# Kernel optimization log

Measured on AMD Instinct MI355X. Metric: run time of the kernel, lower is better.

## Reference

```python
import jax, jax.numpy as jnp
import numpy as np

BATCH, SEQ_LEN, EMBED_DIM = 32, 2048, 128
N_QLAYERS = 2
N_WIRES = 18  # ceil(log2(128*2048)) ; 2**18 == 128*2048 exactly


def rot_matrices(p):
    # p: [n_wires, 3] (phi, theta, omega) -> [n_wires, 2, 2] complex64
    # PennyLane/torchquantum Rot convention: RZ(omega) RY(theta) RZ(phi)
    phi, th, om = p[..., 0], p[..., 1], p[..., 2]
    c, s = jnp.cos(th / 2), jnp.sin(th / 2)
    e = lambda a: jnp.exp(1j * a)  # float32 -> complex64 (weak complex scalar)
    m00 = e(-(phi + om) / 2) * c
    m01 = -e((phi - om) / 2) * s
    m10 = e(-(phi - om) / 2) * s
    m11 = e((phi + om) / 2) * c
    return jnp.stack([jnp.stack([m00, m01], -1), jnp.stack([m10, m11], -1)], -2)


def apply_1q(state, U, w):
    # state: [B, 2^n] complex; wire 0 is the most-significant qubit axis
    B = state.shape[0]
    L, R = 2 ** w, 2 ** (N_WIRES - 1 - w)
    s = state.reshape(B, L, 2, R)
    s = jnp.einsum('ij,bljr->blir', U, s)
    return s.reshape(B, -1)


def apply_cnot(state, c, t):
    # flip target bit t where control bit c == 1
    B = state.shape[0]
    s = state.reshape((B,) + (2,) * N_WIRES)
    ca, ta = c + 1, t + 1
    s0 = jnp.take(s, 0, axis=ca)
    s1 = jnp.take(s, 1, axis=ca)
    flip_axis = ta - 1 if ta > ca else ta  # target axis index after removing control axis
    s1 = jnp.flip(s1, axis=flip_axis)
    return jnp.stack([s0, s1], axis=ca).reshape(B, -1)


def setup_inputs() -> dict:
    key = jax.random.key(0)
    k1, k2 = jax.random.split(key)
    x = jax.random.normal(k1, (BATCH, SEQ_LEN, EMBED_DIM), dtype=jnp.float32)
    params = jax.random.uniform(k2, (N_QLAYERS, N_WIRES, 3), dtype=jnp.float32,
                                minval=-np.pi, maxval=np.pi)
    return {"x": x, "params": params}


def reference(x, params):
    B = x.shape[0]
    v = x.reshape(B, -1)
    # StateEncoder: L2-normalize amplitudes (2^N_WIRES == SEQ_LEN*EMBED_DIM, no padding needed)
    v = v / jnp.sqrt(jnp.sum(v * v, axis=-1, keepdims=True))
    state = v.astype(jnp.complex64)
    for l in range(N_QLAYERS):
        U = rot_matrices(params[l])  # [N_WIRES, 2, 2]
        for w in range(N_WIRES):
            state = apply_1q(state, U[w], w)
        for i in range(N_WIRES):
            state = apply_cnot(state, (i + l) % N_WIRES, (i + l + 1) % N_WIRES)
    return jnp.abs(state).reshape(B, SEQ_LEN, EMBED_DIM)
```

## Files before the change

kernel.cpp:

```cpp
#include <hip/hip_runtime.h>
#include <hip/hip_fp16.h>

#define NW 18
#define NSTATE (1u << NW)
#define NBATCH 32
#define TOTAL (NBATCH * (size_t)NSTATE)

typedef float v2f __attribute__((ext_vector_type(2)));
typedef _Float16 h2v __attribute__((ext_vector_type(2)));

struct Masks { unsigned m[18]; };

__device__ __forceinline__ v2f pk_mulsw(v2f g, v2f b) {
    v2f d;
    asm("v_pk_mul_f32 %0, %1, %2 op_sel:[1,1] op_sel_hi:[1,0] neg_lo:[1,0]"
        : "=v"(d) : "v"(g), "v"(b));
    return d;
}
__device__ __forceinline__ v2f pk_fmare(v2f g, v2f a, v2f c) {
    v2f d;
    asm("v_pk_fma_f32 %0, %1, %2, %3 op_sel:[0,0,0] op_sel_hi:[0,1,1]"
        : "=v"(d) : "v"(g), "v"(a), "v"(c));
    return d;
}
__device__ __forceinline__ v2f pk_fmasw(v2f g, v2f a, v2f c) {
    v2f d;
    asm("v_pk_fma_f32 %0, %1, %2, %3 op_sel:[1,1,0] op_sel_hi:[1,0,1] neg_lo:[1,0,0]"
        : "=v"(d) : "v"(g), "v"(a), "v"(c));
    return d;
}
__device__ __forceinline__ v2f cmul(v2f g, v2f x) { return pk_fmare(g, x, pk_mulsw(g, x)); }
__device__ __forceinline__ v2f cmad(v2f g, v2f x, v2f c) { return pk_fmare(g, x, pk_fmasw(g, x, c)); }

__device__ __forceinline__ void bfly(v2f& a, v2f& b, v2f g00, v2f g01, v2f g10, v2f g11) {
    v2f na = cmad(g00, a, cmul(g01, b));
    v2f nb = cmad(g10, a, cmul(g11, b));
    a = na; b = nb;
}

__device__ __forceinline__ unsigned pack(v2f v) {
    return __builtin_bit_cast(unsigned, __builtin_amdgcn_cvt_pkrtz(v.x, v.y));
}
__device__ __forceinline__ v2f unpack(unsigned u) {
    h2v h = __builtin_bit_cast(h2v, u);
    return (v2f){(float)h.x, (float)h.y};
}

__device__ __forceinline__ int swz(int n) { return n ^ ((n >> 5) & 31); }

__device__ __forceinline__ constexpr int ctzc(int x) {
    int c = 0; while (!(x & 1)) { x >>= 1; c++; } return c;
}

#define GATES(gb)                                                      \
    const float4 G0_ = Ut[(17-(gb))*2+0], G1_ = Ut[(17-(gb))*2+1];     \
    const v2f g00 = {G0_.x, G0_.y}, g01 = {G0_.z, G0_.w};              \
    const v2f g10 = {G1_.x, G1_.y}, g11 = {G1_.z, G1_.w};

__device__ __forceinline__ void make_gate(const float* __restrict__ p,
                                          float4& G0, float4& G1) {
    float phi = p[0], th = p[1], om = p[2];
    float ch = cosf(th*0.5f), sh = sinf(th*0.5f);
    float a0 = -0.5f*(phi+om), a1 = 0.5f*(phi-om);
    float c0 = cosf(a0), s0 = sinf(a0);
    float c1 = cosf(a1), s1 = sinf(a1);
    G0 = make_float4(c0*ch,  s0*ch, -c1*sh, -s1*sh);
    G1 = make_float4(c1*sh, -s1*sh,  c0*ch, -s0*ch);
}

template<int FIRST>
__global__ __launch_bounds__(256, 6) void passA(const void* __restrict__ src,
                                                unsigned* __restrict__ dst,
                                                float4* __restrict__ Utab,
                                                float* __restrict__ partials,
                                                const float* __restrict__ params,
                                                int layer) {
    __shared__ unsigned sm[4096];
    __shared__ float4 gl[72];
    __shared__ float wsum[4];
    const int t = threadIdx.x;
    const size_t base = (size_t)blockIdx.x * 4096;
    v2f v[16];
    const float4* Ut;
    float ss = 0.f;

    if (FIRST) {
        const float4* xs = (const float4*)((const float*)src + base + (size_t)t * 16);

        if (t < 36) {
            float4 G0, G1;
            make_gate(params + t*3, G0, G1);
            gl[t*2] = G0; gl[t*2+1] = G1;
            if (blockIdx.x == 0) { Utab[t*2] = G0; Utab[t*2+1] = G1; }
        }

#pragma unroll
        for (int j = 0; j < 4; j++) {
            float4 q = xs[j];
            v[j*4+0] = (v2f){q.x, 0.f};
            v[j*4+1] = (v2f){q.y, 0.f};
            v[j*4+2] = (v2f){q.z, 0.f};
            v[j*4+3] = (v2f){q.w, 0.f};
            ss += q.x*q.x + q.y*q.y + q.z*q.z + q.w*q.w;
        }
#pragma unroll
        for (int m = 32; m >= 1; m >>= 1) ss += __shfl_xor(ss, m, 64);
        if ((t & 63) == 0) wsum[t >> 6] = ss;
        __syncthreads();
        Ut = gl;
    } else {
        const uint4* xs = (const uint4*)((const unsigned*)src + base + (size_t)t * 16);
#pragma unroll
        for (int j = 0; j < 4; j++) {
            uint4 q = xs[j];
            v[j*4+0] = unpack(q.x);
            v[j*4+1] = unpack(q.y);
            v[j*4+2] = unpack(q.z);
            v[j*4+3] = unpack(q.w);
        }
        Ut = (const float4*)Utab + (size_t)layer * 36;
    }

#pragma unroll
    for (int b = 0; b < 4; b++) {
        GATES(b);
#pragma unroll
        for (int k = 0; k < 16; k++)
            if (!(k & (1 << b))) bfly(v[k], v[k | (1 << b)], g00, g01, g10, g11);
    }

#pragma unroll
    for (int k = 0; k < 16; k++)
        sm[swz((t << 4) | k)] = pack(v[k]);
    __syncthreads();
    if (FIRST && t == 0)
        partials[blockIdx.x] = wsum[0] + wsum[1] + wsum[2] + wsum[3];
#pragma unroll
    for (int k = 0; k < 16; k++)
        v[k] = unpack(sm[swz((t & 15) | (k << 4) | ((t >> 4) << 8))]);

#pragma unroll
    for (int b = 4; b < 8; b++) {
        GATES(b);
        const int pb = 1 << (b - 4);
#pragma unroll
        for (int k = 0; k < 16; k++)
            if (!(k & pb)) bfly(v[k], v[k | pb], g00, g01, g10, g11);
    }

#pragma unroll
    for (int k = 0; k < 16; k++)
        sm[swz((t & 15) | (k << 4) | ((t >> 4) << 8))] = pack(v[k]);
    __syncthreads();
#pragma unroll
    for (int k = 0; k < 16; k++)
        v[k] = unpack(sm[swz(t | (k << 8))]);

#pragma unroll
    for (int b = 8; b < 12; b++) {
        GATES(b);
        const int pb = 1 << (b - 8);
#pragma unroll
        for (int k = 0; k < 16; k++)
            if (!(k & pb)) bfly(v[k], v[k | pb], g00, g01, g10, g11);
    }

#pragma unroll
    for (int k = 0; k < 16; k++)
        dst[base + (t | (k << 8))] = pack(v[k]);
}

template<int LAST>
__global__ __launch_bounds__(256, 6) void passB(const unsigned* __restrict__ src,
                                                void* __restrict__ dst,
                                                const float4* __restrict__ Utab,
                                                const float* __restrict__ partials,
                                                int layer, Masks mk) {
    __shared__ unsigned sm[4096];
    const int t = threadIdx.x;
    const unsigned blk = blockIdx.x;
    const unsigned batch = blk >> 6;
    const unsigned chunk = blk & 63;
    const unsigned low = chunk * 64 + (t & 63);
    const unsigned j = t >> 6;
    const size_t bb = (size_t)batch << NW;

    v2f v[16];
#pragma unroll
    for (int k = 0; k < 16; k++) {
        unsigned h = (j << 4) | k;
        v[k] = unpack(src[bb + ((size_t)h << 12) + low]);
    }

    const float4* Ut = Utab + (size_t)layer * 36;
#pragma unroll
    for (int b = 12; b < 16; b++) {
        GATES(b);
        const int pb = 1 << (b - 12);
#pragma unroll
        for (int k = 0; k < 16; k++)
            if (!(k & pb)) bfly(v[k], v[k | pb], g00, g01, g10, g11);
    }

#pragma unroll
    for (int k = 0; k < 16; k++) {
        unsigned h = (j << 4) | k;
        sm[(h << 6) | (t & 63)] = pack(v[k]);
    }
    __syncthreads();
#pragma unroll
    for (int q = 0; q < 4; q++)
#pragma unroll
        for (int r = 0; r < 4; r++) {
            unsigned h = (q << 4) | (j << 2) | r;
            v[(q << 2) | r] = unpack(sm[(h << 6) | (t & 63)]);
        }

    {
        GATES(16);
#pragma unroll
        for (int k = 0; k < 16; k++)
            if (!(k & 4)) bfly(v[k], v[k | 4], g00, g01, g10, g11);
    }
    {
        GATES(17);
#pragma unroll
        for (int k = 0; k < 16; k++)
            if (!(k & 8)) bfly(v[k], v[k | 8], g00, g01, g10, g11);
    }

    unsigned f = 0;
#pragma unroll
    for (int kk = 0; kk < 12; kk++) f ^= ((low >> kk) & 1u) ? mk.m[kk] : 0u;
    if (j & 1) f ^= mk.m[14];
    if (j & 2) f ^= mk.m[15];

    float sc = 1.f;
    if (LAST) {
        float nrm = 0.f;
#pragma unroll
        for (int i = 0; i < 64; i++) nrm += partials[batch * 64 + i];
        sc = rsqrtf(nrm);
    }

    const unsigned gm0 = mk.m[12], gm1 = mk.m[13], gm2 = mk.m[16], gm3 = mk.m[17];
    unsigned fs = f;
#pragma unroll
    for (int i = 0; i < 16; i++) {
        if (i) {
            const int c = ctzc(i);
            fs ^= (c == 0) ? gm0 : (c == 1) ? gm1 : (c == 2) ? gm2 : gm3;
        }
        const int s = i ^ (i >> 1);
        if (LAST) {
            ((float*)dst)[bb + fs] = sc * sqrtf(fmaf(v[s].x, v[s].x, v[s].y*v[s].y));
        } else {
            ((unsigned*)dst)[bb + fs] = pack(v[s]);
        }
    }
}

static void chain_masks(int l, Masks* mk) {
    unsigned rows[18];
    for (int j = 0; j < 18; j++) rows[j] = 1u << j;
    for (int i = 0; i < 18; i++) {
        int cw = (i + l) % 18, tw = (i + l + 1) % 18;
        rows[17 - tw] ^= rows[17 - cw];
    }
    for (int k = 0; k < 18; k++) {
        unsigned cm = 0;
        for (int j = 0; j < 18; j++) cm |= ((rows[j] >> k) & 1u) << j;
        mk->m[k] = cm;
    }
}

extern "C" void kernel_launch(void* const* d_in, const int* in_sizes, int n_in,
                              void* d_out, int out_size, void* d_ws, size_t ws_size,
                              hipStream_t stream) {
    const float* x      = (const float*)d_in[0];
    const float* params = (const float*)d_in[1];

    char* ws = (char*)d_ws;
    unsigned* bufA  = (unsigned*)ws;
    unsigned* bufB  = (unsigned*)(ws + TOTAL * 4);
    float4*   Utab  = (float4*)(ws + TOTAL * 8);
    float* partials = (float*)(ws + TOTAL * 8 + 4096);

    Masks mk1, mk2;
    chain_masks(0, &mk1);
    chain_masks(1, &mk2);

    passA<1><<<2048, 256, 0, stream>>>((const void*)x, bufA, Utab, partials, params, 0);
    passB<0><<<2048, 256, 0, stream>>>(bufA, (void*)bufB, Utab, partials, 0, mk1);
    passA<0><<<2048, 256, 0, stream>>>((const void*)bufB, bufB, Utab, partials, params, 1);
    passB<1><<<2048, 256, 0, stream>>>(bufB, d_out, Utab, partials, 1, mk2);
}
```

Measured before the change: 157.9 us.

## Fuse quantum circuit into three passes by commuting CNOT permutation across layer-2 gates

Reorganises the two-layer circuit from four kernels into three. Layer 1's high-wire gates and some of layer 2's gates now run in one middle pass, with the CNOT-chain permutation folded into gate-pair selection through parity-dependent gate swaps and a prefix-XOR index remap. A final pass applies the remaining layer-2 gates, applies the combined permutation, and writes magnitudes. This removes one full read and write of the fp16-packed state, at the cost of more complex index arithmetic, runtime gate selection, and a lower occupancy hint in the launch bounds.

```diff
diff --git a/kernel.cpp b/kernel.cpp
--- a/kernel.cpp
+++ b/kernel.cpp
@@ -10,6 +10,7 @@
 typedef _Float16 h2v __attribute__((ext_vector_type(2)));
 
 struct Masks { unsigned m[18]; };
+struct G4 { v2f a, b, c, d; };
 
 __device__ __forceinline__ v2f pk_mulsw(v2f g, v2f b) {
     v2f d;
@@ -32,10 +33,22 @@
 __device__ __forceinline__ v2f cmul(v2f g, v2f x) { return pk_fmare(g, x, pk_mulsw(g, x)); }
 __device__ __forceinline__ v2f cmad(v2f g, v2f x, v2f c) { return pk_fmare(g, x, pk_fmasw(g, x, c)); }
 
-__device__ __forceinline__ void bfly(v2f& a, v2f& b, v2f g00, v2f g01, v2f g10, v2f g11) {
-    v2f na = cmad(g00, a, cmul(g01, b));
-    v2f nb = cmad(g10, a, cmul(g11, b));
-    a = na; b = nb;
+__device__ __forceinline__ void bflyG(v2f& x, v2f& y, const G4 g) {
+    v2f nx = cmad(g.a, x, cmul(g.b, y));
+    v2f ny = cmad(g.c, x, cmul(g.d, y));
+    x = nx; y = ny;
+}
+
+__device__ __forceinline__ G4 loadg(const float4* __restrict__ Ut, int gb) {
+    float4 G0 = Ut[(17 - gb) * 2], G1 = Ut[(17 - gb) * 2 + 1];
+    G4 g; g.a = (v2f){G0.x, G0.y}; g.b = (v2f){G0.z, G0.w};
+    g.c = (v2f){G1.x, G1.y}; g.d = (v2f){G1.z, G1.w};
+    return g;
+}
+__device__ __forceinline__ G4 selg(const G4 g, unsigned p) {
+    G4 r; r.a = p ? g.d : g.a; r.b = p ? g.c : g.b;
+    r.c = p ? g.b : g.c; r.d = p ? g.a : g.d;
+    return r;
 }
 
 __device__ __forceinline__ unsigned pack(v2f v) {
@@ -47,107 +60,93 @@
 }
 
 __device__ __forceinline__ int swz(int n) { return n ^ ((n >> 5) & 31); }
+#define SWZ2(L) ((unsigned)(L) ^ (((((unsigned)(L)) >> 5) ^ (((unsigned)(L)) >> 6)) & 1u))
 
 __device__ __forceinline__ constexpr int ctzc(int x) {
     int c = 0; while (!(x & 1)) { x >>= 1; c++; } return c;
 }
-
-#define GATES(gb)                                                      \
-    const float4 G0_ = Ut[(17-(gb))*2+0], G1_ = Ut[(17-(gb))*2+1];     \
-    const v2f g00 = {G0_.x, G0_.y}, g01 = {G0_.z, G0_.w};              \
-    const v2f g10 = {G1_.x, G1_.y}, g11 = {G1_.z, G1_.w};
+__device__ __forceinline__ unsigned pfx18(unsigned x) {
+    x ^= x << 1; x ^= x << 2; x ^= x << 4; x ^= x << 8; x ^= x << 16;
+    return x & 0x3FFFFu;
+}
 
 __device__ __forceinline__ void make_gate(const float* __restrict__ p,
                                           float4& G0, float4& G1) {
     float phi = p[0], th = p[1], om = p[2];
-    float ch = cosf(th*0.5f), sh = sinf(th*0.5f);
-    float a0 = -0.5f*(phi+om), a1 = 0.5f*(phi-om);
+    float ch = cosf(th * 0.5f), sh = sinf(th * 0.5f);
+    float a0 = -0.5f * (phi + om), a1 = 0.5f * (phi - om);
     float c0 = cosf(a0), s0 = sinf(a0);
     float c1 = cosf(a1), s1 = sinf(a1);
-    G0 = make_float4(c0*ch,  s0*ch, -c1*sh, -s1*sh);
-    G1 = make_float4(c1*sh, -s1*sh,  c0*ch, -s0*ch);
-}
-
-template<int FIRST>
-__global__ __launch_bounds__(256, 6) void passA(const void* __restrict__ src,
+    G0 = make_float4(c0 * ch, s0 * ch, -c1 * sh, -s1 * sh);
+    G1 = make_float4(c1 * sh, -s1 * sh, c0 * ch, -s0 * ch);
+}
+
+__global__ __launch_bounds__(256, 4) void pass1(const float* __restrict__ src,
                                                 unsigned* __restrict__ dst,
                                                 float4* __restrict__ Utab,
                                                 float* __restrict__ partials,
-                                                const float* __restrict__ params,
-                                                int layer) {
+                                                const float* __restrict__ params) {
     __shared__ unsigned sm[4096];
-    __shared__ float4 gl[72];
+    __shared__ float4 gl[36];
     __shared__ float wsum[4];
     const int t = threadIdx.x;
     const size_t base = (size_t)blockIdx.x * 4096;
     v2f v[16];
-    const float4* Ut;
     float ss = 0.f;
 
-    if (FIRST) {
-        const float4* xs = (const float4*)((const float*)src + base + (size_t)t * 16);
-
-        if (t < 36) {
-            float4 G0, G1;
-            make_gate(params + t*3, G0, G1);
-            gl[t*2] = G0; gl[t*2+1] = G1;
-            if (blockIdx.x == 0) { Utab[t*2] = G0; Utab[t*2+1] = G1; }
+    const float4* xs = (const float4*)(src + base + (size_t)t * 16);
+
+    if (t < 36) {
+        float4 G0, G1; make_gate(params + t * 3, G0, G1);
+        if (t < 18) { gl[t * 2] = G0; gl[t * 2 + 1] = G1; }
+        if (blockIdx.x == 0) {
+            Utab[t * 2] = G0; Utab[t * 2 + 1] = G1;
+            if (t >= 18) {
+                Utab[72 + (t - 18) * 2 + 0] = make_float4(G1.z, G1.w, G1.x, G1.y);
+                Utab[72 + (t - 18) * 2 + 1] = make_float4(G0.z, G0.w, G0.x, G0.y);
+            }
         }
-
-#pragma unroll
-        for (int j = 0; j < 4; j++) {
-            float4 q = xs[j];
-            v[j*4+0] = (v2f){q.x, 0.f};
-            v[j*4+1] = (v2f){q.y, 0.f};
-            v[j*4+2] = (v2f){q.z, 0.f};
-            v[j*4+3] = (v2f){q.w, 0.f};
-            ss += q.x*q.x + q.y*q.y + q.z*q.z + q.w*q.w;
-        }
-#pragma unroll
-        for (int m = 32; m >= 1; m >>= 1) ss += __shfl_xor(ss, m, 64);
-        if ((t & 63) == 0) wsum[t >> 6] = ss;
-        __syncthreads();
-        Ut = gl;
-    } else {
-        const uint4* xs = (const uint4*)((const unsigned*)src + base + (size_t)t * 16);
-#pragma unroll
-        for (int j = 0; j < 4; j++) {
-            uint4 q = xs[j];
-            v[j*4+0] = unpack(q.x);
-            v[j*4+1] = unpack(q.y);
-            v[j*4+2] = unpack(q.z);
-            v[j*4+3] = unpack(q.w);
-        }
-        Ut = (const float4*)Utab + (size_t)layer * 36;
-    }
+    }
+
+#pragma unroll
+    for (int j = 0; j < 4; j++) {
+        float4 q = xs[j];
+        v[j * 4 + 0] = (v2f){q.x, 0.f};
+        v[j * 4 + 1] = (v2f){q.y, 0.f};
+        v[j * 4 + 2] = (v2f){q.z, 0.f};
+        v[j * 4 + 3] = (v2f){q.w, 0.f};
+        ss += q.x * q.x + q.y * q.y + q.z * q.z + q.w * q.w;
+    }
+#pragma unroll
+    for (int m = 32; m >= 1; m >>= 1) ss += __shfl_xor(ss, m, 64);
+    if ((t & 63) == 0) wsum[t >> 6] = ss;
+    __syncthreads();
+
+    const float4* Ut = gl;
 
 #pragma unroll
     for (int b = 0; b < 4; b++) {
-        GATES(b);
-#pragma unroll
-        for (int k = 0; k < 16; k++)
-            if (!(k & (1 << b))) bfly(v[k], v[k | (1 << b)], g00, g01, g10, g11);
-    }
-
+        G4 g = loadg(Ut, b);
+#pragma unroll
+        for (int k = 0; k < 16; k++)
+            if (!(k & (1 << b))) bflyG(v[k], v[k | (1 << b)], g);
+    }
 #pragma unroll
     for (int k = 0; k < 16; k++)
         sm[swz((t << 4) | k)] = pack(v[k]);
     __syncthreads();
-    if (FIRST && t == 0)
-        partials[blockIdx.x] = wsum[0] + wsum[1] + wsum[2] + wsum[3];
+    if (t == 0) partials[blockIdx.x] = wsum[0] + wsum[1] + wsum[2] + wsum[3];
 #pragma unroll
     for (int k = 0; k < 16; k++)
         v[k] = unpack(sm[swz((t & 15) | (k << 4) | ((t >> 4) << 8))]);
-
 #pragma unroll
     for (int b = 4; b < 8; b++) {
-        GATES(b);
+        G4 g = loadg(Ut, b);
         const int pb = 1 << (b - 4);
 #pragma unroll
         for (int k = 0; k < 16; k++)
-            if (!(k & pb)) bfly(v[k], v[k | pb], g00, g01, g10, g11);
-    }
-
+            if (!(k & pb)) bflyG(v[k], v[k | pb], g);
+    }
 #pragma unroll
     for (int k = 0; k < 16; k++)
         sm[swz((t & 15) | (k << 4) | ((t >> 4) << 8))] = pack(v[k]);
@@ -155,122 +154,231 @@
 #pragma unroll
     for (int k = 0; k < 16; k++)
         v[k] = unpack(sm[swz(t | (k << 8))]);
-
 #pragma unroll
     for (int b = 8; b < 12; b++) {
-        GATES(b);
+        G4 g = loadg(Ut, b);
         const int pb = 1 << (b - 8);
 #pragma unroll
         for (int k = 0; k < 16; k++)
-            if (!(k & pb)) bfly(v[k], v[k | pb], g00, g01, g10, g11);
-    }
-
+            if (!(k & pb)) bflyG(v[k], v[k | pb], g);
+    }
 #pragma unroll
     for (int k = 0; k < 16; k++)
         dst[base + (t | (k << 8))] = pack(v[k]);
 }
 
-template<int LAST>
-__global__ __launch_bounds__(256, 6) void passB(const unsigned* __restrict__ src,
-                                                void* __restrict__ dst,
-                                                const float4* __restrict__ Utab,
-                                                const float* __restrict__ partials,
-                                                int layer, Masks mk) {
+__global__ __launch_bounds__(256, 4) void pass2(const unsigned* __restrict__ src,
+                                                unsigned* __restrict__ dst,
+                                                const float4* __restrict__ Utab) {
     __shared__ unsigned sm[4096];
     const int t = threadIdx.x;
     const unsigned blk = blockIdx.x;
-    const unsigned batch = blk >> 6;
-    const unsigned chunk = blk & 63;
-    const unsigned low = chunk * 64 + (t & 63);
-    const unsigned j = t >> 6;
+    const unsigned batch = blk >> 6, chunk = blk & 63;
     const size_t bb = (size_t)batch << NW;
-
+    const int lane6 = t & 63, j2 = t >> 6;
+    const float4* Ut0  = Utab;
+    const float4* Ut1  = Utab + 36;
+    const float4* Ut1s = Utab + 72;
     v2f v[16];
+
+#pragma unroll
+    for (int k = 0; k < 16; k++)
+        v[k] = unpack(src[bb + ((size_t)((j2 << 4) | k) << 12) + (chunk << 6) + lane6]);
+
+#pragma unroll
+    for (int b = 0; b < 4; b++) {
+        G4 g = loadg(Ut0, 12 + b);
+#pragma unroll
+        for (int k = 0; k < 16; k++)
+            if (!(k & (1 << b))) bflyG(v[k], v[k | (1 << b)], g);
+    }
+
+#pragma unroll
+    for (int k = 0; k < 16; k++)
+        sm[SWZ2((((j2 << 4) | k) << 6) | lane6)] = pack(v[k]);
+    __syncthreads();
+    const int l5 = t & 31, m3 = t >> 5;
 #pragma unroll
     for (int k = 0; k < 16; k++) {
-        unsigned h = (j << 4) | k;
-        v[k] = unpack(src[bb + ((size_t)h << 12) + low]);
-    }
-
-    const float4* Ut = Utab + (size_t)layer * 36;
-#pragma unroll
-    for (int b = 12; b < 16; b++) {
-        GATES(b);
-        const int pb = 1 << (b - 12);
-#pragma unroll
-        for (int k = 0; k < 16; k++)
-            if (!(k & pb)) bfly(v[k], v[k | pb], g00, g01, g10, g11);
-    }
+        int L = ((((k >> 3) << 5) | (((k >> 2) & 1) << 4) | (((k >> 1) & 1) << 3) | m3) << 6)
+                | (l5 << 1) | (k & 1);
+        v[k] = unpack(sm[SWZ2(L)]);
+    }
+
+    { G4 g = loadg(Ut0, 16);
+#pragma unroll
+      for (int k = 0; k < 16; k++) if (!(k & 4)) bflyG(v[k], v[k | 4], g); }
+    { G4 g = loadg(Ut0, 17);
+#pragma unroll
+      for (int k = 0; k < 16; k++) if (!(k & 8)) bflyG(v[k], v[k | 8], g); }
+
+    { G4 g = loadg(Ut1, 16);
+#pragma unroll
+      for (int k = 0; k < 16; k++) if (!(k & 2)) {
+          const int q = k ^ 6, pe = ((k >> 2) ^ (k >> 3)) & 1;
+          if (pe) bflyG(v[q], v[k], g); else bflyG(v[k], v[q], g);
+      } }
+
+    const unsigned ptv = (unsigned)((__popc(l5) + __popc((int)chunk) + __popc(m3)) & 1);
+
+    { G4 gn = loadg(Ut1, 17);
+      G4 cA = selg(gn, ptv), cB = selg(gn, ptv ^ 1u);
+#pragma unroll
+      for (int k = 0; k < 16; k++) if (!(k & 4)) {
+          const int q = k ^ 12, pe = (k ^ (k >> 1) ^ (k >> 2)) & 1;
+          bflyG(v[k], v[q], pe ? cB : cA);
+      } }
+
+    { G4 gn = loadg(Ut1, 0);
+      G4 cA = selg(gn, ptv), cB = selg(gn, ptv ^ 1u);
+#pragma unroll
+      for (int k = 0; k < 16; k++) if (!(k & 1)) {
+          const int q = k ^ 13, pe = (k ^ (k >> 1) ^ (k >> 2) ^ (k >> 3)) & 1;
+          bflyG(v[k], v[q], pe ? cB : cA);
+      } }
 
 #pragma unroll
     for (int k = 0; k < 16; k++) {
-        unsigned h = (j << 4) | k;
-        sm[(h << 6) | (t & 63)] = pack(v[k]);
-    }
-    __syncthreads();
-#pragma unroll
-    for (int q = 0; q < 4; q++)
-#pragma unroll
-        for (int r = 0; r < 4; r++) {
-            unsigned h = (q << 4) | (j << 2) | r;
-            v[(q << 2) | r] = unpack(sm[(h << 6) | (t & 63)]);
-        }
-
-    {
-        GATES(16);
-#pragma unroll
-        for (int k = 0; k < 16; k++)
-            if (!(k & 4)) bfly(v[k], v[k | 4], g00, g01, g10, g11);
-    }
-    {
-        GATES(17);
-#pragma unroll
-        for (int k = 0; k < 16; k++)
-            if (!(k & 8)) bfly(v[k], v[k | 8], g00, g01, g10, g11);
-    }
-
-    unsigned f = 0;
-#pragma unroll
-    for (int kk = 0; kk < 12; kk++) f ^= ((low >> kk) & 1u) ? mk.m[kk] : 0u;
-    if (j & 1) f ^= mk.m[14];
-    if (j & 2) f ^= mk.m[15];
-
-    float sc = 1.f;
-    if (LAST) {
-        float nrm = 0.f;
-#pragma unroll
-        for (int i = 0; i < 64; i++) nrm += partials[batch * 64 + i];
-        sc = rsqrtf(nrm);
-    }
-
-    const unsigned gm0 = mk.m[12], gm1 = mk.m[13], gm2 = mk.m[16], gm3 = mk.m[17];
-    unsigned fs = f;
+        int L = ((((k >> 3) << 5) | (((k >> 2) & 1) << 4) | (((k >> 1) & 1) << 3) | m3) << 6)
+                | (l5 << 1) | (k & 1);
+        sm[SWZ2(L)] = pack(v[k]);
+    }
+    __syncthreads();
+#pragma unroll
+    for (int k = 0; k < 16; k++)
+        v[k] = unpack(sm[SWZ2((((j2 << 4) | k) << 6) | lane6)]);
+
+    const unsigned pt3 = (unsigned)((j2 ^ (j2 >> 1)) & 1);
+    const float4* U3 = pt3 ? Ut1s : Ut1;
+    { G4 g = loadg(U3, 13);
+#pragma unroll
+      for (int k = 0; k < 16; k++) if (!(k & 1)) {
+          const int q = k ^ 3, pe = ((k >> 1) ^ (k >> 2) ^ (k >> 3)) & 1;
+          if (pe) bflyG(v[q], v[k], g); else bflyG(v[k], v[q], g);
+      } }
+    { G4 g = loadg(U3, 14);
+#pragma unroll
+      for (int k = 0; k < 16; k++) if (!(k & 2)) {
+          const int q = k ^ 6, pe = ((k >> 2) ^ (k >> 3)) & 1;
+          if (pe) bflyG(v[q], v[k], g); else bflyG(v[k], v[q], g);
+      } }
+    { G4 g = loadg(U3, 15);
+#pragma unroll
+      for (int k = 0; k < 16; k++) if (!(k & 4)) {
+          const int q = k ^ 12, pe = (k >> 3) & 1;
+          if (pe) bflyG(v[q], v[k], g); else bflyG(v[k], v[q], g);
+      } }
+
+    const unsigned fixedx = ((unsigned)j2 << 16) | (chunk << 6) | (unsigned)lane6;
+    unsigned us = pfx18(fixedx);
 #pragma unroll
     for (int i = 0; i < 16; i++) {
         if (i) {
             const int c = ctzc(i);
-            fs ^= (c == 0) ? gm0 : (c == 1) ? gm1 : (c == 2) ? gm2 : gm3;
+            us ^= (c == 0) ? 0x3F000u : (c == 1) ? 0x3E000u : (c == 2) ? 0x3C000u : 0x38000u;
         }
         const int s = i ^ (i >> 1);
-        if (LAST) {
-            ((float*)dst)[bb + fs] = sc * sqrtf(fmaf(v[s].x, v[s].x, v[s].y*v[s].y));
-        } else {
-            ((unsigned*)dst)[bb + fs] = pack(v[s]);
+        dst[bb + us] = pack(v[s]);
+    }
+}
+
+__global__ __launch_bounds__(256, 4) void pass3(const unsigned* __restrict__ src,
+                                                float* __restrict__ out,
+                                                const float4* __restrict__ Utab,
+                                                const float* __restrict__ partials,
+                                                Masks W) {
+    __shared__ unsigned sm[4096];
+    const int t = threadIdx.x;
+    const unsigned blk = blockIdx.x;
+    const unsigned batch = blk >> 6, loc = blk & 63;
+    const size_t bb = (size_t)batch << NW;
+    const size_t base = bb + ((size_t)loc << 12);
+    const unsigned u17 = (loc >> 5) & 1;
+    const float4* Ut = Utab + (u17 ? 72 : 36);
+    v2f v[16];
+
+    const uint4* xs = (const uint4*)(src + base + (size_t)t * 16);
+#pragma unroll
+    for (int j = 0; j < 4; j++) {
+        uint4 q = xs[j];
+        v[j * 4 + 0] = unpack(q.x);
+        v[j * 4 + 1] = unpack(q.y);
+        v[j * 4 + 2] = unpack(q.z);
+        v[j * 4 + 3] = unpack(q.w);
+    }
+
+#pragma unroll
+    for (int b = 0; b < 4; b++) {
+        G4 g = loadg(Ut, b + 1);
+#pragma unroll
+        for (int k = 0; k < 16; k++)
+            if (!(k & (1 << b))) bflyG(v[k], v[k | (1 << b)], g);
+    }
+#pragma unroll
+    for (int k = 0; k < 16; k++)
+        sm[swz((t << 4) | k)] = pack(v[k]);
+    __syncthreads();
+#pragma unroll
+    for (int k = 0; k < 16; k++)
+        v[k] = unpack(sm[swz((t & 15) | (k << 4) | ((t >> 4) << 8))]);
+#pragma unroll
+    for (int b = 4; b < 8; b++) {
+        G4 g = loadg(Ut, b + 1);
+        const int pb = 1 << (b - 4);
+#pragma unroll
+        for (int k = 0; k < 16; k++)
+            if (!(k & pb)) bflyG(v[k], v[k | pb], g);
+    }
+#pragma unroll
+    for (int k = 0; k < 16; k++)
+        sm[swz((t & 15) | (k << 4) | ((t >> 4) << 8))] = pack(v[k]);
+    __syncthreads();
+#pragma unroll
+    for (int k = 0; k < 16; k++)
+        v[k] = unpack(sm[swz(t | (k << 8))]);
+#pragma unroll
+    for (int b = 8; b < 12; b++) {
+        G4 g = loadg(Ut, b + 1);
+        const int pb = 1 << (b - 8);
+#pragma unroll
+        for (int k = 0; k < 16; k++)
+            if (!(k & pb)) bflyG(v[k], v[k | pb], g);
+    }
+
+    float nrm = 0.f;
+#pragma unroll
+    for (int i = 0; i < 64; i++) nrm += partials[batch * 64 + i];
+    const float sc = rsqrtf(nrm);
+
+    unsigned f = 0;
+    const unsigned fx = (loc << 12) | (unsigned)t;
+#pragma unroll
+    for (int i = 0; i < 18; i++) {
+        if (i >= 8 && i < 12) continue;
+        if ((fx >> i) & 1) f ^= W.m[i];
+    }
+    unsigned fs = f;
+#pragma unroll
+    for (int i = 0; i < 16; i++) {
+        if (i) fs ^= W.m[8 + ctzc(i)];
+        const int s = i ^ (i >> 1);
+        out[bb + fs] = sc * sqrtf(fmaf(v[s].x, v[s].x, v[s].y * v[s].y));
+    }
+}
+
+static unsigned apply_m(const unsigned* col, unsigned x) {
+    unsigned r = 0;
+    for (int i = 0; i < 18; i++) if ((x >> i) & 1) r ^= col[i];
+    return r;
+}
+static void perm_cols(int l, unsigned* col) {
+    for (int i = 0; i < 18; i++) {
+        unsigned x = 1u << i;
+        for (int g = 0; g < 18; g++) {
+            int cb = 17 - ((g + l) % 18), tb = 17 - ((g + l + 1) % 18);
+            if ((x >> cb) & 1) x ^= 1u << tb;
         }
-    }
-}
-
-static void chain_masks(int l, Masks* mk) {
-    unsigned rows[18];
-    for (int j = 0; j < 18; j++) rows[j] = 1u << j;
-    for (int i = 0; i < 18; i++) {
-        int cw = (i + l) % 18, tw = (i + l + 1) % 18;
-        rows[17 - tw] ^= rows[17 - cw];
-    }
-    for (int k = 0; k < 18; k++) {
-        unsigned cm = 0;
-        for (int j = 0; j < 18; j++) cm |= ((rows[j] >> k) & 1u) << j;
-        mk->m[k] = cm;
+        col[i] = x;
     }
 }
 
@@ -286,12 +394,16 @@
     float4*   Utab  = (float4*)(ws + TOTAL * 8);
     float* partials = (float*)(ws + TOTAL * 8 + 4096);
 
-    Masks mk1, mk2;
-    chain_masks(0, &mk1);
-    chain_masks(1, &mk2);
-
-    passA<1><<<2048, 256, 0, stream>>>((const void*)x, bufA, Utab, partials, params, 0);
-    passB<0><<<2048, 256, 0, stream>>>(bufA, (void*)bufB, Utab, partials, 0, mk1);
-    passA<0><<<2048, 256, 0, stream>>>((const void*)bufB, bufB, Utab, partials, params, 1);
-    passB<1><<<2048, 256, 0, stream>>>(bufB, d_out, Utab, partials, 1, mk2);
-}
+    unsigned P1c[18], P2c[18];
+    perm_cols(0, P1c);
+    perm_cols(1, P2c);
+    Masks W;
+    for (int k = 0; k < 18; k++) {
+        unsigned tinv = (1u << k) | (k < 17 ? (1u << (k + 1)) : 0u);
+        W.m[k] = apply_m(P2c, apply_m(P1c, tinv));
+    }
+
+    pass1<<<2048, 256, 0, stream>>>(x, bufA, Utab, partials, params);
+    pass2<<<2048, 256, 0, stream>>>(bufA, bufB, Utab);
+    pass3<<<2048, 256, 0, stream>>>(bufB, (float*)d_out, Utab, partials, W);
+}
```

Result: faster. 147.1 us (-6.9%).
